# Performance work log

Measured on AMD Instinct MI355X. Metric: run time of the kernel, lower is better.

Reference implementation:

```python
import jax, jax.numpy as jnp
import numpy as np

B, T, DM = 2, 512, 1024
H, DH = 16, 64          # n_heads, d_head = d_model // n_heads
D, R = 32, 4            # d_manifold, metric_net rank
TEMP_MIN = 0.5


def _rope_tables(t_len, d_head):
    inv_freq = 1.0 / (10000.0 ** (jnp.arange(0, d_head, 2, dtype=jnp.float32) / d_head))
    t = jnp.arange(t_len, dtype=jnp.float32)
    freqs = t[:, None] * inv_freq[None, :]          # [T, d_head//2]
    emb = jnp.concatenate([freqs, freqs], axis=-1)  # [T, d_head]
    return jnp.cos(emb), jnp.sin(emb)


def _apply_rope(x, cos, sin):
    # x: [B, H, T, d_head]
    half = x.shape[-1] // 2
    x1, x2 = x[..., :half], x[..., half:]
    c1 = cos[None, None, :, :half]
    s1 = sin[None, None, :, :half]
    return jnp.concatenate([x1 * c1 - x2 * s1, x1 * s1 + x2 * c1], axis=-1)


def setup_inputs() -> dict:
    key = jax.random.key(0)
    ks = jax.random.split(key, 9)
    s = 0.02
    return {
        "x": jax.random.normal(ks[0], (B, T, DM), dtype=jnp.float32),
        "Wq": s * jax.random.normal(ks[1], (DM, DM), dtype=jnp.float32),
        "Wk": s * jax.random.normal(ks[2], (DM, DM), dtype=jnp.float32),
        "Wv": s * jax.random.normal(ks[3], (DM, DM), dtype=jnp.float32),
        "Wo": s * jax.random.normal(ks[4], (DM, DM), dtype=jnp.float32),
        "Wqm": s * jax.random.normal(ks[5], (DH, D), dtype=jnp.float32),
        "Wkm": s * jax.random.normal(ks[6], (DH, D), dtype=jnp.float32),
        "Wmetric": s * jax.random.normal(ks[7], (D, D * R), dtype=jnp.float32),
        "temperature": jnp.asarray(1.0, dtype=jnp.float32),
    }


def reference(x, Wq, Wk, Wv, Wo, Wqm, Wkm, Wmetric, temperature):
    b, t, c = x.shape
    # projections -> [B, H, T, d_head]
    def split_heads(y):
        return y.reshape(b, t, H, DH).transpose(0, 2, 1, 3)
    q = split_heads(x @ Wq)
    k = split_heads(x @ Wk)
    v = split_heads(x @ Wv)

    cos, sin = _rope_tables(t, DH)
    q = _apply_rope(q, cos, sin)
    k = _apply_rope(k, cos, sin)

    # manifold coordinates in (0,1): [B, H, T, D]
    qm = jax.nn.sigmoid(jnp.einsum('bhtd,dm->bhtm', q, Wqm))
    km = jax.nn.sigmoid(jnp.einsum('bhtd,dm->bhtm', k, Wkm))

    # low-rank metric factor U(q): [B, H, T, D, R]
    U = jnp.einsum('bhtm,mn->bhtn', qm, Wmetric).reshape(b, H, t, D, R)

    # Euclidean part: ||q_i - k_j||^2 = |q|^2 + |k|^2 - 2 q.k  -> [B,H,T,T]
    q2 = jnp.sum(qm * qm, axis=-1)
    k2 = jnp.sum(km * km, axis=-1)
    qk = jnp.einsum('bhid,bhjd->bhij', qm, km)
    dist_euc = q2[..., :, None] + k2[..., None, :] - 2.0 * qk

    # low-rank part: ||U_i^T (q_i - k_j)||^2, factorized as U_i^T q_i - U_i^T k_j
    Uq = jnp.einsum('bhidr,bhid->bhir', U, qm)          # [B,H,T,R]
    Uk = jnp.einsum('bhidr,bhjd->bhijr', U, km)         # [B,H,T,T,R]
    dist_lr = jnp.sum((Uq[:, :, :, None, :] - Uk) ** 2, axis=-1)

    dist_sq = jnp.maximum(dist_euc + dist_lr, 0.0)

    temp = jnp.maximum(temperature, TEMP_MIN)
    attn = -dist_sq / temp

    causal = jnp.triu(jnp.ones((t, t), dtype=bool), k=1)
    attn = jnp.where(causal[None, None], -jnp.inf, attn)
    attn = jax.nn.softmax(attn, axis=-1)

    out = jnp.einsum('bhij,bhjd->bhid', attn, v)        # [B,H,T,d_head]
    out = out.transpose(0, 2, 1, 3).reshape(b, t, c)
    return out @ Wo
```

## Files before the change

kernel.cpp:

```cpp
#include <hip/hip_runtime.h>
#include <cmath>

constexpr int B_  = 2;
constexpr int T_  = 512;
constexpr int DM_ = 1024;
constexpr int H_  = 16;
constexpr int DH_ = 64;
constexpr int D_  = 32;
constexpr int R_  = 4;
constexpr int BH_ = B_ * H_;

typedef __bf16 bf16x8 __attribute__((ext_vector_type(8)));
typedef float  f32x4  __attribute__((ext_vector_type(4)));
typedef unsigned short u16x8 __attribute__((ext_vector_type(8)));

__device__ __forceinline__ unsigned short f2bf(float f) {
    unsigned u = __float_as_uint(f);
    return (unsigned short)((u + 0x7fffu + ((u >> 16) & 1u)) >> 16);
}
__device__ __forceinline__ float bf2f(unsigned short v) {
    return __uint_as_float((unsigned)v << 16);
}
__device__ __forceinline__ void gload16(const void* g, void* l) {
    __builtin_amdgcn_global_load_lds(
        (const __attribute__((address_space(1))) void*)g,
        (__attribute__((address_space(3))) void*)l, 16, 0, 0);
}

__global__ __launch_bounds__(256) void prep_kernel(
    const float* __restrict__ x,
    const float* __restrict__ Wq, const float* __restrict__ Wk,
    const float* __restrict__ Wv, const float* __restrict__ Wo,
    unsigned short* __restrict__ xb,
    unsigned short* __restrict__ wqb, unsigned short* __restrict__ wkb,
    unsigned short* __restrict__ wvb, unsigned short* __restrict__ wob)
{
    const int t = threadIdx.x;
    const int z = blockIdx.z;
    if (z == 4) {
        int base = (blockIdx.y * 16 + blockIdx.x) * 4096 + t * 16;
#pragma unroll
        for (int c = 0; c < 4; ++c) {
            float4 v = *(const float4*)&x[base + c * 4];
            ushort4 o = { f2bf(v.x), f2bf(v.y), f2bf(v.z), f2bf(v.w) };
            *(ushort4*)&xb[base + c * 4] = o;
        }
        return;
    }
    __shared__ __align__(16) unsigned short Ls[64][72];
    const float* W = (z == 0) ? Wq : (z == 1) ? Wk : (z == 2) ? Wv : Wo;
    unsigned short* O = (z == 0) ? wqb : (z == 1) ? wkb : (z == 2) ? wvb : wob;
    const int k0 = blockIdx.x * 64;
    const int n0 = blockIdx.y * 64;
#pragma unroll
    for (int it = 0; it < 4; ++it) {
        int r = it * 16 + (t >> 4);
        int c = (t & 15) * 4;
        float4 v4 = *(const float4*)&W[(size_t)(k0 + r) * DM_ + n0 + c];
        Ls[c + 0][r] = f2bf(v4.x); Ls[c + 1][r] = f2bf(v4.y);
        Ls[c + 2][r] = f2bf(v4.z); Ls[c + 3][r] = f2bf(v4.w);
    }
    __syncthreads();
#pragma unroll
    for (int it = 0; it < 2; ++it) {
        int nl = it * 32 + (t >> 3);
        int kc = (t & 7) * 8;
        *(u16x8*)&O[(size_t)(n0 + nl) * DM_ + k0 + kc] = *(const u16x8*)&Ls[nl][kc];
    }
}

template <int EPI>
__global__ __launch_bounds__(256) void mfma_gemm_db(
    const unsigned short* __restrict__ A,
    const unsigned short* __restrict__ Bt0,
    const unsigned short* __restrict__ Bt1,
    const unsigned short* __restrict__ Bt2,
    float* __restrict__ C0, float* __restrict__ C1,
    unsigned short* __restrict__ vT)
{
    __shared__ __align__(16) unsigned short As[3][64 * 64];
    __shared__ __align__(16) unsigned short Bs[3][64 * 64];
    const int tid  = threadIdx.x;
    const int lane = tid & 63;
    const int w    = tid >> 6;
    const int wm   = (w & 1) * 32;
    const int wn   = (w >> 1) * 32;
    const int l15  = lane & 15, quad = lane >> 4;

    const int bm = blockIdx.y * 64;
    int bn, which = 0;
    const unsigned short* Bt;
    if (EPI == 0) {
        int n0 = blockIdx.x * 64;
        which = n0 >> 10;
        bn = n0 & 1023;
        Bt = (which == 0) ? Bt0 : (which == 1) ? Bt1 : Bt2;
    } else {
        bn = blockIdx.x * 64;
        Bt = Bt0;
    }

    const int srow = tid >> 3, kcs = tid & 7, kcg = kcs ^ (srow & 7);
    const unsigned short* Ap0 = A  + (size_t)(bm + srow) * DM_ + kcg * 8;
    const unsigned short* Bp0 = Bt + (size_t)(bn + srow) * DM_ + kcg * 8;
    const unsigned short* Ap1 = Ap0 + 32 * DM_;
    const unsigned short* Bp1 = Bp0 + 32 * DM_;

    gload16(Ap0, &As[0][tid * 8]);
    gload16(Ap1, &As[0][tid * 8 + 2048]);
    gload16(Bp0, &Bs[0][tid * 8]);
    gload16(Bp1, &Bs[0][tid * 8 + 2048]);
    gload16(Ap0 + 64, &As[1][tid * 8]);
    gload16(Ap1 + 64, &As[1][tid * 8 + 2048]);
    gload16(Bp0 + 64, &Bs[1][tid * 8]);
    gload16(Bp1 + 64, &Bs[1][tid * 8 + 2048]);

    f32x4 acc[2][2] = {};
#pragma unroll
    for (int k = 0; k < 16; ++k) {
        const int cur = k % 3, pre = (k + 2) % 3;
        __builtin_amdgcn_s_barrier();
        if (k + 2 < 16) {
            const int off = (k + 2) * 64;
            gload16(Ap0 + off, &As[pre][tid * 8]);
            gload16(Ap1 + off, &As[pre][tid * 8 + 2048]);
            gload16(Bp0 + off, &Bs[pre][tid * 8]);
            gload16(Bp1 + off, &Bs[pre][tid * 8 + 2048]);
            __builtin_amdgcn_s_waitcnt(0x0F78);
        } else if (k + 1 < 16) {
            __builtin_amdgcn_s_waitcnt(0x0F74);
        } else {
            __builtin_amdgcn_s_waitcnt(0x0F70);
        }
        __builtin_amdgcn_s_barrier();

        bf16x8 af[2][2], bfr[2][2];
#pragma unroll
        for (int ki = 0; ki < 2; ++ki)
#pragma unroll
            for (int i = 0; i < 2; ++i) {
                int ra = wm + i * 16 + l15;
                int rb = wn + i * 16 + l15;
                int kch = ki * 4 + quad;
                af[ki][i]  = *(const bf16x8*)&As[cur][ra * 64 + (kch ^ (ra & 7)) * 8];
                bfr[ki][i] = *(const bf16x8*)&Bs[cur][rb * 64 + (kch ^ (rb & 7)) * 8];
            }
#pragma unroll
        for (int mi = 0; mi < 2; ++mi)
#pragma unroll
            for (int ni = 0; ni < 2; ++ni) {
                acc[mi][ni] = __builtin_amdgcn_mfma_f32_16x16x32_bf16(
                    af[0][mi], bfr[0][ni], acc[mi][ni], 0, 0, 0);
                acc[mi][ni] = __builtin_amdgcn_mfma_f32_16x16x32_bf16(
                    af[1][mi], bfr[1][ni], acc[mi][ni], 0, 0, 0);
            }
    }

#pragma unroll
    for (int mi = 0; mi < 2; ++mi)
#pragma unroll
        for (int ni = 0; ni < 2; ++ni) {
            f32x4 a = acc[mi][ni];
            int col = wn + ni * 16 + l15;
#pragma unroll
            for (int r = 0; r < 4; ++r) {
                int row = bm + wm + mi * 16 + quad * 4 + r;
                if (EPI == 0) {
                    int h = bn >> 6, d = col;
                    int bb = row >> 9, tt = row & (T_ - 1);
                    if (which == 2) {
                        vT[(((size_t)bb * H_ + h) * DH_ + d) * T_ + tt] = f2bf(a[r]);
                    } else {
                        float* C = (which == 0) ? C0 : C1;
                        C[(((size_t)bb * H_ + h) * T_ + tt) * DH_ + d] = a[r];
                    }
                } else {
                    C0[(size_t)row * DM_ + bn + col] = a[r];
                }
            }
        }
}

__global__ __launch_bounds__(256) void feat_both(
    const float* __restrict__ q_raw, const float* __restrict__ k_raw,
    const float* __restrict__ Wqm,   const float* __restrict__ Wkm,
    const float* __restrict__ Wmetric,
    unsigned short* __restrict__ a_hi, unsigned short* __restrict__ a_lo,
    unsigned short* __restrict__ km_hi, unsigned short* __restrict__ km_lo,
    float* __restrict__ q2p, float* __restrict__ k2,
    unsigned short* __restrict__ Urb)
{
    const bool QSIDE = (blockIdx.y == 0);
    const float* raw = QSIDE ? q_raw : k_raw;
    const float* Wm  = QSIDE ? Wqm   : Wkm;

    __shared__ float qrs[4][64];
    __shared__ float qms[4][32];
    const int tid  = threadIdx.x;
    const int w    = tid >> 6;
    const int lane = tid & 63;
    const int row  = blockIdx.x * 4 + w;
    const int t    = row & (T_ - 1);
    const int bh   = row >> 9;

    const int m  = lane & 31;
    const int hh = lane >> 5;

    float rv = raw[(size_t)row * 64 + lane];
    float ang = (float)t * expf((float)m * -0.28782313662425575f);
    float s, c;
    sincosf(ang, &s, &c);
    float partner = __shfl_xor(rv, 32);
    float qr = (lane < 32) ? (rv * c - partner * s) : (partner * s + rv * c);
    qrs[w][lane] = qr;

    float acc = 0.f;
#pragma unroll 8
    for (int i = 0; i < 32; ++i) {
        int d = hh * 32 + i;
        acc += qrs[w][d] * Wm[d * 32 + m];
    }
    acc += __shfl_xor(acc, 32);
    const float qm = 1.0f / (1.0f + __expf(-acc));
    if (hh == 0) qms[w][m] = qm;

    if (!QSIDE) {
        if (lane < 32) {
            unsigned short hi = f2bf(qm);
            unsigned short lo = f2bf(qm - bf2f(hi));
            size_t off = (size_t)row * 32 + lane;
            km_hi[off] = hi; km_lo[off] = lo;
        }
        float sq = (lane < 32) ? qm * qm : 0.f;
        sq += __shfl_xor(sq, 32); sq += __shfl_xor(sq, 16);
        sq += __shfl_xor(sq, 8);  sq += __shfl_xor(sq, 4);
        sq += __shfl_xor(sq, 2);  sq += __shfl_xor(sq, 1);
        if (lane == 0) k2[row] = sq;
        return;
    }

    float a0 = 0.f, a1 = 0.f;
#pragma unroll 8
    for (int mm = 0; mm < 32; ++mm) {
        float qv = qms[w][mm];
        float2 wv = *(const float2*)&Wmetric[mm * 128 + lane * 2];
        a0 += qv * wv.x;
        a1 += qv * wv.y;
    }

    {
        int n0i = lane * 2;
        int r0 = n0i & 3, d0 = n0i >> 2;
        Urb[(((size_t)bh * R_ + r0    ) * T_ + t) * D_ + d0] = f2bf(a0);
        Urb[(((size_t)bh * R_ + r0 + 1) * T_ + t) * D_ + d0] = f2bf(a1);
    }

    float dq = qms[w][lane >> 1];
    float u0 = a0 * dq, u1 = a1 * dq;
    u0 += __shfl_xor(u0, 2);  u1 += __shfl_xor(u1, 2);
    u0 += __shfl_xor(u0, 4);  u1 += __shfl_xor(u1, 4);
    u0 += __shfl_xor(u0, 8);  u1 += __shfl_xor(u1, 8);
    u0 += __shfl_xor(u0, 16); u1 += __shfl_xor(u1, 16);
    u0 += __shfl_xor(u0, 32); u1 += __shfl_xor(u1, 32);
    float v0 = __shfl_xor(u0, 1), v1 = __shfl_xor(u1, 1);
    const bool odd = (lane & 1);
    float Uq0 = odd ? v0 : u0;
    float Uq1 = odd ? v1 : u1;
    float Uq2 = odd ? u0 : v0;
    float Uq3 = odd ? u1 : v1;

    {
        int src = m * 2;
        float s0 = __shfl(a0, src);
        float s1 = __shfl(a1, src);
        float s2 = __shfl(a0, src + 1);
        float s3 = __shfl(a1, src + 1);
        if (lane < 32) {
            float b = Uq0 * s0 + Uq1 * s1 + Uq2 * s2 + Uq3 * s3;
            float a = qm + b;
            unsigned short hi = f2bf(a);
            unsigned short lo = f2bf(a - bf2f(hi));
            size_t off = (size_t)row * 32 + lane;
            a_hi[off] = hi; a_lo[off] = lo;
        }
    }

    float sq = (lane < 32) ? qm * qm : 0.f;
    sq += __shfl_xor(sq, 32); sq += __shfl_xor(sq, 16);
    sq += __shfl_xor(sq, 8);  sq += __shfl_xor(sq, 4);
    sq += __shfl_xor(sq, 2);  sq += __shfl_xor(sq, 1);
    if (lane == 0)
        q2p[row] = sq + Uq0 * Uq0 + Uq1 * Uq1 + Uq2 * Uq2 + Uq3 * Uq3;
}

constexpr int PROW = 40;
__global__ __launch_bounds__(256) void attn_mfma(
    const unsigned short* __restrict__ a_hi, const unsigned short* __restrict__ a_lo,
    const unsigned short* __restrict__ km_hi, const unsigned short* __restrict__ km_lo,
    const unsigned short* __restrict__ Urb,
    const float* __restrict__ q2p, const float* __restrict__ k2,
    const float* __restrict__ temp_p, const unsigned short* __restrict__ vT,
    unsigned short* __restrict__ ctxb)
{
    __shared__ __align__(16) unsigned short P_lds[4][32 * PROW];
    __shared__ __align__(16) float OP[4][32][64];
    __shared__ float ML[4][32];

    const int itile = blockIdx.x, bh = blockIdx.y;
    const int i0 = itile * 32;
    const int tid = threadIdx.x, w = tid >> 6, lane = tid & 63;
    const int l15 = lane & 15, quad = lane >> 4;

    const float inv_temp = 1.0f / fmaxf(temp_p[0], 0.5f);

    bf16x8 Ahi[2], Alo[2], Aur[4][2];
#pragma unroll
    for (int mi = 0; mi < 2; ++mi) {
        size_t ab = ((size_t)bh * T_ + i0 + mi * 16 + l15) * 32 + quad * 8;
        Ahi[mi] = *(const bf16x8*)&a_hi[ab];
        Alo[mi] = *(const bf16x8*)&a_lo[ab];
#pragma unroll
        for (int r = 0; r < 4; ++r)
            Aur[r][mi] = *(const bf16x8*)
                &Urb[(((size_t)bh * R_ + r) * T_ + i0 + mi * 16 + l15) * 32 + quad * 8];
    }
    float q2r[2][4];
#pragma unroll
    for (int mi = 0; mi < 2; ++mi)
#pragma unroll
        for (int rg = 0; rg < 4; ++rg)
            q2r[mi][rg] = q2p[(size_t)bh * T_ + i0 + mi * 16 + quad * 4 + rg];

    f32x4 Oacc[2][4] = {};
    float psum[2][4] = {};

    for (int jt = w; jt <= itile; jt += 4) {
        const int j0 = jt * 32;
        bf16x8 Bhi[2], Blo[2];
#pragma unroll
        for (int ni = 0; ni < 2; ++ni) {
            size_t kb = ((size_t)bh * T_ + j0 + ni * 16 + l15) * 32 + quad * 8;
            Bhi[ni] = *(const bf16x8*)&km_hi[kb];
            Blo[ni] = *(const bf16x8*)&km_lo[kb];
        }
        f32x4 acc[2][2] = {};
#pragma unroll
        for (int mi = 0; mi < 2; ++mi)
#pragma unroll
            for (int ni = 0; ni < 2; ++ni) {
                acc[mi][ni] = __builtin_amdgcn_mfma_f32_16x16x32_bf16(
                    Alo[mi], Bhi[ni], acc[mi][ni], 0, 0, 0);
                acc[mi][ni] = __builtin_amdgcn_mfma_f32_16x16x32_bf16(
                    Ahi[mi], Blo[ni], acc[mi][ni], 0, 0, 0);
                acc[mi][ni] = __builtin_amdgcn_mfma_f32_16x16x32_bf16(
                    Ahi[mi], Bhi[ni], acc[mi][ni], 0, 0, 0);
            }
        f32x4 sq[2][2] = {};
#pragma unroll
        for (int r = 0; r < 4; ++r) {
            f32x4 ar[2][2] = {};
#pragma unroll
            for (int mi = 0; mi < 2; ++mi)
#pragma unroll
                for (int ni = 0; ni < 2; ++ni)
                    ar[mi][ni] = __builtin_amdgcn_mfma_f32_16x16x32_bf16(
                        Aur[r][mi], Bhi[ni], ar[mi][ni], 0, 0, 0);
#pragma unroll
            for (int mi = 0; mi < 2; ++mi)
#pragma unroll
                for (int ni = 0; ni < 2; ++ni)
                    sq[mi][ni] += ar[mi][ni] * ar[mi][ni];
        }
        float k2c[2];
#pragma unroll
        for (int ni = 0; ni < 2; ++ni)
            k2c[ni] = k2[(size_t)bh * T_ + j0 + ni * 16 + l15];
        const bool diag = (jt == itile);
#pragma unroll
        for (int mi = 0; mi < 2; ++mi)
#pragma unroll
            for (int ni = 0; ni < 2; ++ni)
#pragma unroll
                for (int rg = 0; rg < 4; ++rg) {
                    float dist = q2r[mi][rg] + k2c[ni]
                               - 2.f * acc[mi][ni][rg] + sq[mi][ni][rg];
                    float sc = -fmaxf(dist, 0.f) * inv_temp;
                    if (diag && (ni * 16 + l15) > (mi * 16 + quad * 4 + rg))
                        sc = -1e30f;
                    float p = __expf(sc);
                    psum[mi][rg] += p;
                    P_lds[w][(mi * 16 + quad * 4 + rg) * PROW + ni * 16 + l15] = f2bf(p);
                }
        bf16x8 Pf[2], Vf[4];
#pragma unroll
        for (int mi = 0; mi < 2; ++mi)
            Pf[mi] = *(const bf16x8*)&P_lds[w][(mi * 16 + l15) * PROW + quad * 8];
#pragma unroll
        for (int n4 = 0; n4 < 4; ++n4)
            Vf[n4] = *(const bf16x8*)
                &vT[((size_t)bh * DH_ + n4 * 16 + l15) * T_ + j0 + quad * 8];
#pragma unroll
        for (int mi = 0; mi < 2; ++mi)
#pragma unroll
            for (int n4 = 0; n4 < 4; ++n4)
                Oacc[mi][n4] = __builtin_amdgcn_mfma_f32_16x16x32_bf16(
                    Pf[mi], Vf[n4], Oacc[mi][n4], 0, 0, 0);
    }

#pragma unroll
    for (int mi = 0; mi < 2; ++mi)
#pragma unroll
        for (int rg = 0; rg < 4; ++rg) {
            float v = psum[mi][rg];
            v += __shfl_xor(v, 1); v += __shfl_xor(v, 2);
            v += __shfl_xor(v, 4); v += __shfl_xor(v, 8);
            psum[mi][rg] = v;
        }
    if (l15 == 0)
#pragma unroll
        for (int mi = 0; mi < 2; ++mi)
#pragma unroll
            for (int rg = 0; rg < 4; ++rg)
                ML[w][mi * 16 + quad * 4 + rg] = psum[mi][rg];
#pragma unroll
    for (int mi = 0; mi < 2; ++mi)
#pragma unroll
        for (int n4 = 0; n4 < 4; ++n4)
#pragma unroll
            for (int rg = 0; rg < 4; ++rg)
                OP[w][mi * 16 + quad * 4 + rg][n4 * 16 + l15] = Oacc[mi][n4][rg];
    __syncthreads();

    const int ii = tid >> 3, ds = tid & 7;
    float l = ML[0][ii] + ML[1][ii] + ML[2][ii] + ML[3][ii];
    float O[8] = {};
#pragma unroll
    for (int wv = 0; wv < 4; ++wv) {
        float4 o0 = *(const float4*)&OP[wv][ii][ds * 8];
        float4 o1 = *(const float4*)&OP[wv][ii][ds * 8 + 4];
        O[0] += o0.x; O[1] += o0.y; O[2] += o0.z; O[3] += o0.w;
        O[4] += o1.x; O[5] += o1.y; O[6] += o1.z; O[7] += o1.w;
    }
    const float inv = 1.0f / l;
    const int b = bh >> 4, h = bh & 15;
    u16x8 o;
#pragma unroll
    for (int dd = 0; dd < 8; ++dd) o[dd] = f2bf(O[dd] * inv);
    *(u16x8*)&ctxb[((size_t)b * T_ + i0 + ii) * DM_ + h * 64 + ds * 8] = o;
}

extern "C" void kernel_launch(void* const* d_in, const int* in_sizes, int n_in,
                              void* d_out, int out_size, void* d_ws, size_t ws_size,
                              hipStream_t stream)
{
    const float* x       = (const float*)d_in[0];
    const float* Wq      = (const float*)d_in[1];
    const float* Wk      = (const float*)d_in[2];
    const float* Wv      = (const float*)d_in[3];
    const float* Wo      = (const float*)d_in[4];
    const float* Wqm     = (const float*)d_in[5];
    const float* Wkm     = (const float*)d_in[6];
    const float* Wmetric = (const float*)d_in[7];
    const float* temp    = (const float*)d_in[8];
    float* out = (float*)d_out;
    float* ws  = (float*)d_ws;

    float* q_raw = ws;
    float* k_raw = q_raw + (size_t)BH_ * T_ * DH_;
    float* q2p   = k_raw + (size_t)BH_ * T_ * DH_;
    float* k2    = q2p   + (size_t)BH_ * T_;
    unsigned short* xb   = (unsigned short*)(k2 + (size_t)BH_ * T_);
    unsigned short* wqb  = xb   + (size_t)DM_ * DM_;
    unsigned short* wkb  = wqb  + (size_t)DM_ * DM_;
    unsigned short* wvb  = wkb  + (size_t)DM_ * DM_;
    unsigned short* wob  = wvb  + (size_t)DM_ * DM_;
    unsigned short* a_hi = wob  + (size_t)DM_ * DM_;
    unsigned short* a_lo = a_hi + (size_t)BH_ * T_ * D_;
    unsigned short* kmhi = a_lo + (size_t)BH_ * T_ * D_;
    unsigned short* kmlo = kmhi + (size_t)BH_ * T_ * D_;
    unsigned short* Urb  = kmlo + (size_t)BH_ * T_ * D_;
    unsigned short* vT   = Urb  + (size_t)BH_ * R_ * T_ * D_;
    unsigned short* ctxb = (unsigned short*)q_raw;

    prep_kernel<<<dim3(16, 16, 5), 256, 0, stream>>>(
        x, Wq, Wk, Wv, Wo, xb, wqb, wkb, wvb, wob);
    mfma_gemm_db<0><<<dim3(48, 16), 256, 0, stream>>>(
        xb, wqb, wkb, wvb, q_raw, k_raw, vT);
    feat_both<<<dim3(BH_ * T_ / 4, 2), 256, 0, stream>>>(
        q_raw, k_raw, Wqm, Wkm, Wmetric,
        a_hi, a_lo, kmhi, kmlo, q2p, k2, Urb);
    attn_mfma<<<dim3(T_ / 32, BH_), 256, 0, stream>>>(
        a_hi, a_lo, kmhi, kmlo, Urb, q2p, k2, temp, vT, ctxb);
    mfma_gemm_db<1><<<dim3(16, 16), 256, 0, stream>>>(
        ctxb, wob, nullptr, nullptr, out, nullptr, nullptr);
}
```

Measured before the change: 145.7 us.

## Fuse RoPE and manifold feature computation into QKV GEMM epilogue

```diff
diff --git a/kernel.cpp b/kernel.cpp
--- a/kernel.cpp
+++ b/kernel.cpp
@@ -75,8 +75,14 @@
     const unsigned short* __restrict__ Bt0,
     const unsigned short* __restrict__ Bt1,
     const unsigned short* __restrict__ Bt2,
-    float* __restrict__ C0, float* __restrict__ C1,
-    unsigned short* __restrict__ vT)
+    float* __restrict__ C0,
+    unsigned short* __restrict__ vT,
+    const float* __restrict__ Wqm, const float* __restrict__ Wkm,
+    const float* __restrict__ Wmetric,
+    unsigned short* __restrict__ a_hi, unsigned short* __restrict__ a_lo,
+    unsigned short* __restrict__ km_hi, unsigned short* __restrict__ km_lo,
+    float* __restrict__ q2p, float* __restrict__ k2,
+    unsigned short* __restrict__ Urb)
 {
     __shared__ __align__(16) unsigned short As[3][64 * 64];
     __shared__ __align__(16) unsigned short Bs[3][64 * 64];
@@ -156,141 +162,153 @@
             }
     }
 
-#pragma unroll
-    for (int mi = 0; mi < 2; ++mi)
-#pragma unroll
-        for (int ni = 0; ni < 2; ++ni) {
-            f32x4 a = acc[mi][ni];
-            int col = wn + ni * 16 + l15;
-#pragma unroll
-            for (int r = 0; r < 4; ++r) {
-                int row = bm + wm + mi * 16 + quad * 4 + r;
-                if (EPI == 0) {
-                    int h = bn >> 6, d = col;
-                    int bb = row >> 9, tt = row & (T_ - 1);
-                    if (which == 2) {
-                        vT[(((size_t)bb * H_ + h) * DH_ + d) * T_ + tt] = f2bf(a[r]);
-                    } else {
-                        float* C = (which == 0) ? C0 : C1;
-                        C[(((size_t)bb * H_ + h) * T_ + tt) * DH_ + d] = a[r];
-                    }
-                } else {
+    if (EPI == 1) {
+#pragma unroll
+        for (int mi = 0; mi < 2; ++mi)
+#pragma unroll
+            for (int ni = 0; ni < 2; ++ni) {
+                f32x4 a = acc[mi][ni];
+                int col = wn + ni * 16 + l15;
+#pragma unroll
+                for (int r = 0; r < 4; ++r) {
+                    int row = bm + wm + mi * 16 + quad * 4 + r;
                     C0[(size_t)row * DM_ + bn + col] = a[r];
                 }
             }
-        }
-}
-
-__global__ __launch_bounds__(256) void feat_both(
-    const float* __restrict__ q_raw, const float* __restrict__ k_raw,
-    const float* __restrict__ Wqm,   const float* __restrict__ Wkm,
-    const float* __restrict__ Wmetric,
-    unsigned short* __restrict__ a_hi, unsigned short* __restrict__ a_lo,
-    unsigned short* __restrict__ km_hi, unsigned short* __restrict__ km_lo,
-    float* __restrict__ q2p, float* __restrict__ k2,
-    unsigned short* __restrict__ Urb)
-{
-    const bool QSIDE = (blockIdx.y == 0);
-    const float* raw = QSIDE ? q_raw : k_raw;
-    const float* Wm  = QSIDE ? Wqm   : Wkm;
-
-    __shared__ float qrs[4][64];
-    __shared__ float qms[4][32];
-    const int tid  = threadIdx.x;
-    const int w    = tid >> 6;
-    const int lane = tid & 63;
-    const int row  = blockIdx.x * 4 + w;
-    const int t    = row & (T_ - 1);
-    const int bh   = row >> 9;
-
+        return;
+    }
+
+    if (which == 2) {
+        const int h = bn >> 6;
+#pragma unroll
+        for (int mi = 0; mi < 2; ++mi)
+#pragma unroll
+            for (int ni = 0; ni < 2; ++ni) {
+                f32x4 a = acc[mi][ni];
+                int d = wn + ni * 16 + l15;
+#pragma unroll
+                for (int r = 0; r < 4; ++r) {
+                    int row = bm + wm + mi * 16 + quad * 4 + r;
+                    int bb = row >> 9, tt = row & (T_ - 1);
+                    vT[(((size_t)bb * H_ + h) * DH_ + d) * T_ + tt] = f2bf(a[r]);
+                }
+            }
+        return;
+    }
+
+    float* Ct  = (float*)&As[0][0];
+    float* QRS = (float*)&Bs[0][0];
+    float* QMS = QRS + 256;
+
+    __syncthreads();
+#pragma unroll
+    for (int mi = 0; mi < 2; ++mi)
+#pragma unroll
+        for (int ni = 0; ni < 2; ++ni) {
+            int col = wn + ni * 16 + l15;
+#pragma unroll
+            for (int r = 0; r < 4; ++r)
+                Ct[(wm + mi * 16 + quad * 4 + r) * 68 + col] = acc[mi][ni][r];
+        }
+    __syncthreads();
+
+    const float* Wm = (which == 0) ? Wqm : Wkm;
     const int m  = lane & 31;
     const int hh = lane >> 5;
-
-    float rv = raw[(size_t)row * 64 + lane];
-    float ang = (float)t * expf((float)m * -0.28782313662425575f);
-    float s, c;
-    sincosf(ang, &s, &c);
-    float partner = __shfl_xor(rv, 32);
-    float qr = (lane < 32) ? (rv * c - partner * s) : (partner * s + rv * c);
-    qrs[w][lane] = qr;
-
-    float acc = 0.f;
+    const int h  = bn >> 6;
+
+    for (int rr = 0; rr < 16; ++rr) {
+        const int lrow = w * 16 + rr;
+        const int grow = bm + lrow;
+        const int tt = grow & (T_ - 1), bb = grow >> 9;
+        const int bh = bb * H_ + h;
+        const int frow = bh * T_ + tt;
+
+        float rv = Ct[lrow * 68 + lane];
+        float ang = (float)tt * expf((float)m * -0.28782313662425575f);
+        float s, c;
+        sincosf(ang, &s, &c);
+        float partner = __shfl_xor(rv, 32);
+        float qr = (lane < 32) ? (rv * c - partner * s) : (partner * s + rv * c);
+        QRS[w * 64 + lane] = qr;
+
+        float acc2 = 0.f;
 #pragma unroll 8
-    for (int i = 0; i < 32; ++i) {
-        int d = hh * 32 + i;
-        acc += qrs[w][d] * Wm[d * 32 + m];
-    }
-    acc += __shfl_xor(acc, 32);
-    const float qm = 1.0f / (1.0f + __expf(-acc));
-    if (hh == 0) qms[w][m] = qm;
-
-    if (!QSIDE) {
-        if (lane < 32) {
-            unsigned short hi = f2bf(qm);
-            unsigned short lo = f2bf(qm - bf2f(hi));
-            size_t off = (size_t)row * 32 + lane;
-            km_hi[off] = hi; km_lo[off] = lo;
-        }
-        float sq = (lane < 32) ? qm * qm : 0.f;
+        for (int i = 0; i < 32; ++i) {
+            int d = hh * 32 + i;
+            acc2 += QRS[w * 64 + d] * Wm[d * 32 + m];
+        }
+        acc2 += __shfl_xor(acc2, 32);
+        const float qmv = 1.0f / (1.0f + __expf(-acc2));
+        if (hh == 0) QMS[w * 32 + m] = qmv;
+
+        if (which == 1) {
+            if (lane < 32) {
+                unsigned short hi = f2bf(qmv);
+                unsigned short lo = f2bf(qmv - bf2f(hi));
+                size_t off = (size_t)frow * 32 + lane;
+                km_hi[off] = hi; km_lo[off] = lo;
+            }
+            float sq = (lane < 32) ? qmv * qmv : 0.f;
+            sq += __shfl_xor(sq, 32); sq += __shfl_xor(sq, 16);
+            sq += __shfl_xor(sq, 8);  sq += __shfl_xor(sq, 4);
+            sq += __shfl_xor(sq, 2);  sq += __shfl_xor(sq, 1);
+            if (lane == 0) k2[frow] = sq;
+            continue;
+        }
+
+        float a0 = 0.f, a1 = 0.f;
+#pragma unroll 8
+        for (int mm = 0; mm < 32; ++mm) {
+            float qv = QMS[w * 32 + mm];
+            float2 wv = *(const float2*)&Wmetric[mm * 128 + lane * 2];
+            a0 += qv * wv.x;
+            a1 += qv * wv.y;
+        }
+        {
+            int n0i = lane * 2;
+            int r0 = n0i & 3, d0 = n0i >> 2;
+            Urb[(((size_t)bh * R_ + r0    ) * T_ + tt) * D_ + d0] = f2bf(a0);
+            Urb[(((size_t)bh * R_ + r0 + 1) * T_ + tt) * D_ + d0] = f2bf(a1);
+        }
+
+        float dq = QMS[w * 32 + (lane >> 1)];
+        float u0 = a0 * dq, u1 = a1 * dq;
+        u0 += __shfl_xor(u0, 2);  u1 += __shfl_xor(u1, 2);
+        u0 += __shfl_xor(u0, 4);  u1 += __shfl_xor(u1, 4);
+        u0 += __shfl_xor(u0, 8);  u1 += __shfl_xor(u1, 8);
+        u0 += __shfl_xor(u0, 16); u1 += __shfl_xor(u1, 16);
+        u0 += __shfl_xor(u0, 32); u1 += __shfl_xor(u1, 32);
+        float v0 = __shfl_xor(u0, 1), v1 = __shfl_xor(u1, 1);
+        const bool odd = (lane & 1);
+        float Uq0 = odd ? v0 : u0;
+        float Uq1 = odd ? v1 : u1;
+        float Uq2 = odd ? u0 : v0;
+        float Uq3 = odd ? u1 : v1;
+
+        {
+            int src = m * 2;
+            float s0 = __shfl(a0, src);
+            float s1 = __shfl(a1, src);
+            float s2 = __shfl(a0, src + 1);
+            float s3 = __shfl(a1, src + 1);
+            if (lane < 32) {
+                float b = Uq0 * s0 + Uq1 * s1 + Uq2 * s2 + Uq3 * s3;
+                float a = qmv + b;
+                unsigned short hi = f2bf(a);
+                unsigned short lo = f2bf(a - bf2f(hi));
+                size_t off = (size_t)frow * 32 + lane;
+                a_hi[off] = hi; a_lo[off] = lo;
+            }
+        }
+
+        float sq = (lane < 32) ? qmv * qmv : 0.f;
         sq += __shfl_xor(sq, 32); sq += __shfl_xor(sq, 16);
         sq += __shfl_xor(sq, 8);  sq += __shfl_xor(sq, 4);
         sq += __shfl_xor(sq, 2);  sq += __shfl_xor(sq, 1);
-        if (lane == 0) k2[row] = sq;
-        return;
-    }
-
-    float a0 = 0.f, a1 = 0.f;
-#pragma unroll 8
-    for (int mm = 0; mm < 32; ++mm) {
-        float qv = qms[w][mm];
-        float2 wv = *(const float2*)&Wmetric[mm * 128 + lane * 2];
-        a0 += qv * wv.x;
-        a1 += qv * wv.y;
-    }
-
-    {
-        int n0i = lane * 2;
-        int r0 = n0i & 3, d0 = n0i >> 2;
-        Urb[(((size_t)bh * R_ + r0    ) * T_ + t) * D_ + d0] = f2bf(a0);
-        Urb[(((size_t)bh * R_ + r0 + 1) * T_ + t) * D_ + d0] = f2bf(a1);
-    }
-
-    float dq = qms[w][lane >> 1];
-    float u0 = a0 * dq, u1 = a1 * dq;
-    u0 += __shfl_xor(u0, 2);  u1 += __shfl_xor(u1, 2);
-    u0 += __shfl_xor(u0, 4);  u1 += __shfl_xor(u1, 4);
-    u0 += __shfl_xor(u0, 8);  u1 += __shfl_xor(u1, 8);
-    u0 += __shfl_xor(u0, 16); u1 += __shfl_xor(u1, 16);
-    u0 += __shfl_xor(u0, 32); u1 += __shfl_xor(u1, 32);
-    float v0 = __shfl_xor(u0, 1), v1 = __shfl_xor(u1, 1);
-    const bool odd = (lane & 1);
-    float Uq0 = odd ? v0 : u0;
-    float Uq1 = odd ? v1 : u1;
-    float Uq2 = odd ? u0 : v0;
-    float Uq3 = odd ? u1 : v1;
-
-    {
-        int src = m * 2;
-        float s0 = __shfl(a0, src);
-        float s1 = __shfl(a1, src);
-        float s2 = __shfl(a0, src + 1);
-        float s3 = __shfl(a1, src + 1);
-        if (lane < 32) {
-            float b = Uq0 * s0 + Uq1 * s1 + Uq2 * s2 + Uq3 * s3;
-            float a = qm + b;
-            unsigned short hi = f2bf(a);
-            unsigned short lo = f2bf(a - bf2f(hi));
-            size_t off = (size_t)row * 32 + lane;
-            a_hi[off] = hi; a_lo[off] = lo;
-        }
-    }
-
-    float sq = (lane < 32) ? qm * qm : 0.f;
-    sq += __shfl_xor(sq, 32); sq += __shfl_xor(sq, 16);
-    sq += __shfl_xor(sq, 8);  sq += __shfl_xor(sq, 4);
-    sq += __shfl_xor(sq, 2);  sq += __shfl_xor(sq, 1);
-    if (lane == 0)
-        q2p[row] = sq + Uq0 * Uq0 + Uq1 * Uq1 + Uq2 * Uq2 + Uq3 * Uq3;
+        if (lane == 0)
+            q2p[frow] = sq + Uq0 * Uq0 + Uq1 * Uq1 + Uq2 * Uq2 + Uq3 * Uq3;
+    }
 }
 
 constexpr int PROW = 40;
@@ -465,11 +483,10 @@
     float* out = (float*)d_out;
     float* ws  = (float*)d_ws;
 
-    float* q_raw = ws;
-    float* k_raw = q_raw + (size_t)BH_ * T_ * DH_;
-    float* q2p   = k_raw + (size_t)BH_ * T_ * DH_;
-    float* k2    = q2p   + (size_t)BH_ * T_;
-    unsigned short* xb   = (unsigned short*)(k2 + (size_t)BH_ * T_);
+    float* q2p = ws;
+    float* k2  = q2p + (size_t)BH_ * T_;
+    unsigned short* ctxb = (unsigned short*)(k2 + (size_t)BH_ * T_);
+    unsigned short* xb   = ctxb + (size_t)B_ * T_ * DM_;
     unsigned short* wqb  = xb   + (size_t)DM_ * DM_;
     unsigned short* wkb  = wqb  + (size_t)DM_ * DM_;
     unsigned short* wvb  = wkb  + (size_t)DM_ * DM_;
@@ -480,17 +497,16 @@
     unsigned short* kmlo = kmhi + (size_t)BH_ * T_ * D_;
     unsigned short* Urb  = kmlo + (size_t)BH_ * T_ * D_;
     unsigned short* vT   = Urb  + (size_t)BH_ * R_ * T_ * D_;
-    unsigned short* ctxb = (unsigned short*)q_raw;
 
     prep_kernel<<<dim3(16, 16, 5), 256, 0, stream>>>(
         x, Wq, Wk, Wv, Wo, xb, wqb, wkb, wvb, wob);
     mfma_gemm_db<0><<<dim3(48, 16), 256, 0, stream>>>(
-        xb, wqb, wkb, wvb, q_raw, k_raw, vT);
-    feat_both<<<dim3(BH_ * T_ / 4, 2), 256, 0, stream>>>(
-        q_raw, k_raw, Wqm, Wkm, Wmetric,
-        a_hi, a_lo, kmhi, kmlo, q2p, k2, Urb);
+        xb, wqb, wkb, wvb, nullptr, vT,
+        Wqm, Wkm, Wmetric, a_hi, a_lo, kmhi, kmlo, q2p, k2, Urb);
     attn_mfma<<<dim3(T_ / 32, BH_), 256, 0, stream>>>(
         a_hi, a_lo, kmhi, kmlo, Urb, q2p, k2, temp, vT, ctxb);
     mfma_gemm_db<1><<<dim3(16, 16), 256, 0, stream>>>(
-        ctxb, wob, nullptr, nullptr, out, nullptr, nullptr);
-}
+        ctxb, wob, nullptr, nullptr, out, nullptr,
+        nullptr, nullptr, nullptr, nullptr, nullptr,
+        nullptr, nullptr, nullptr, nullptr, nullptr);
+}
```

Result: slower. 151.6 us (+4.1%).
